# Performance work log

Hardware: AMD Instinct MI355X
Metric: run time of the kernel (lower is better)

The kernel has to match this reference:

```python
import jax, jax.numpy as jnp
import numpy as np

B, N, M, D, H = 2, 2048, 77, 1024, 16
DH = D // H
SCALE = DH ** -0.5
EPS = 1e-5


def _round_ste(x):
    return x + jax.lax.stop_gradient(jnp.round(x) - x)


def _fq(x, delta, zp, n_bits):
    # UniformAffineQuantizer: fake quant-dequant with straight-through round
    xi = _round_ste(x / delta) + zp
    xq = jnp.clip(xi, 0.0, 2.0 ** n_bits - 1.0)
    return (xq - zp) * delta


def _ln(x, g, b):
    mu = jnp.mean(x, -1, keepdims=True)
    var = jnp.var(x, -1, keepdims=True)
    return (x - mu) * jax.lax.rsqrt(var + EPS) * g + b


def _attn(x, ctx, wq, wk, wv, wo, bo, dq, dk, dv, dw):
    b, n, _ = x.shape
    m = ctx.shape[1]
    q = (x @ wq).reshape(b, n, H, DH).transpose(0, 2, 1, 3)   # b h n d
    k = (ctx @ wk).reshape(b, m, H, DH).transpose(0, 2, 1, 3)
    v = (ctx @ wv).reshape(b, m, H, DH).transpose(0, 2, 1, 3)
    sim = jnp.einsum('bhid,bhjd->bhij', _fq(q, dq, 128.0, 8), _fq(k, dk, 128.0, 8)) * SCALE
    attn = jax.nn.softmax(sim, axis=-1)
    out = jnp.einsum('bhij,bhjd->bhid', _fq(attn, dw, 0.0, 8), _fq(v, dv, 128.0, 8))
    out = out.transpose(0, 2, 1, 3).reshape(b, n, D)
    return out @ wo + bo


def setup_inputs():
    key = jax.random.key(0)
    ks = jax.random.split(key, 16)
    w = lambda k, s: (jax.random.normal(k, s, jnp.float32) * 0.02)
    d = lambda v: jnp.full((1,), v, jnp.float32)
    return {
        'x': jax.random.normal(ks[0], (B, N, D), jnp.float32),
        'context': jax.random.normal(ks[1], (B, M, D), jnp.float32),
        'ln1_g': jnp.ones((D,), jnp.float32), 'ln1_b': jnp.zeros((D,), jnp.float32),
        'ln2_g': jnp.ones((D,), jnp.float32), 'ln2_b': jnp.zeros((D,), jnp.float32),
        'ln3_g': jnp.ones((D,), jnp.float32), 'ln3_b': jnp.zeros((D,), jnp.float32),
        'a1_wq': w(ks[2], (D, D)), 'a1_wk': w(ks[3], (D, D)), 'a1_wv': w(ks[4], (D, D)),
        'a1_wo': w(ks[5], (D, D)), 'a1_bo': jnp.zeros((D,), jnp.float32),
        'a2_wq': w(ks[6], (D, D)), 'a2_wk': w(ks[7], (D, D)), 'a2_wv': w(ks[8], (D, D)),
        'a2_wo': w(ks[9], (D, D)), 'a2_bo': jnp.zeros((D,), jnp.float32),
        'ff_w1': w(ks[10], (D, 8 * D)), 'ff_b1': jnp.zeros((8 * D,), jnp.float32),
        'ff_w2': w(ks[11], (4 * D, D)), 'ff_b2': jnp.zeros((D,), jnp.float32),
        'd_q1': d(0.02), 'd_k1': d(0.02), 'd_v1': d(0.02), 'd_w1': d(1.0 / 255.0),
        'd_q2': d(0.02), 'd_k2': d(0.02), 'd_v2': d(0.02), 'd_w2': d(1.0 / 255.0),
    }


def reference(x, context, ln1_g, ln1_b, ln2_g, ln2_b, ln3_g, ln3_b,
              a1_wq, a1_wk, a1_wv, a1_wo, a1_bo,
              a2_wq, a2_wk, a2_wv, a2_wo, a2_bo,
              ff_w1, ff_b1, ff_w2, ff_b2,
              d_q1, d_k1, d_v1, d_w1, d_q2, d_k2, d_v2, d_w2):
    # x = attn1(norm1(x)) + x   (self-attention)
    h1 = _ln(x, ln1_g, ln1_b)
    x = _attn(h1, h1, a1_wq, a1_wk, a1_wv, a1_wo, a1_bo, d_q1, d_k1, d_v1, d_w1) + x
    # x = attn2(norm2(x), context) + x   (cross-attention)
    h2 = _ln(x, ln2_g, ln2_b)
    x = _attn(h2, context, a2_wq, a2_wk, a2_wv, a2_wo, a2_bo, d_q2, d_k2, d_v2, d_w2) + x
    # x = ff(norm3(x)) + x   (GEGLU feed-forward)
    h3 = _ln(x, ln3_g, ln3_b)
    hg = h3 @ ff_w1 + ff_b1
    a, g = jnp.split(hg, 2, axis=-1)
    x = (a * jax.nn.gelu(g, approximate=False)) @ ff_w2 + ff_b2 + x
    return x
```

## Files before the change

### kernel.cpp

```cpp
#include <hip/hip_runtime.h>
#include <cstdint>
#include <cmath>

typedef unsigned short u16;
typedef unsigned int   u32;

typedef __bf16 bx8 __attribute__((ext_vector_type(8)));
typedef float  fx4 __attribute__((ext_vector_type(4)));
typedef u32    ux4 __attribute__((ext_vector_type(4)));

#define H_  16
#define DH_ 64
#define QSCALE 0.18033688011112042f

#if __has_builtin(__builtin_amdgcn_exp2f)
#define EXP2(x) __builtin_amdgcn_exp2f(x)
#else
#define EXP2(x) exp2f(x)
#endif

__device__ __forceinline__ float bf2f(u16 h){ return __uint_as_float(((u32)h) << 16); }
__device__ __forceinline__ u16 f2bf(float f){
  u32 u = __float_as_uint(f);
  u32 r = (u + 0x7FFFu + ((u >> 16) & 1u)) >> 16;
  return (u16)r;
}

__device__ __forceinline__ u32 pk_bf16(float a, float b){
  u32 r;
  asm("v_cvt_pk_bf16_f32 %0, %1, %2" : "=v"(r) : "v"(a), "v"(b));
  return r;
}

union pkc { ux4 u; bx8 v; };

__device__ __forceinline__ float ldv(const void* p, size_t i, int f32){
  return f32 ? ((const float*)p)[i] : bf2f(((const u16*)p)[i]);
}

__device__ __forceinline__ void gld16(const void* g, void* l){
  __builtin_amdgcn_global_load_lds((const __attribute__((address_space(1))) u32*)g,
                                   (__attribute__((address_space(3))) u32*)l,
                                   16, 0, 0);
}

__device__ __forceinline__ float fq_val(float v, float delta){
  float xi = rintf(v / delta) + 128.0f;
  xi = fminf(fmaxf(xi, 0.0f), 255.0f);
  return (xi - 128.0f) * delta;
}

__device__ __forceinline__ float gelu_f(float x){
  float x3 = x * x * x;
  float z = 0.7978845608028654f * x + 0.035677408136300125f * x3;
  float u = __expf(-2.0f * z);
  float t = 1.0f - 2.0f * u / (1.0f + u);
  return 0.5f * x * (1.0f + t);
}

__global__ void detect_k(const u32* __restrict__ x, int* __restrict__ flag){
  __shared__ int cnt;
  if (threadIdx.x == 0) cnt = 0;
  __syncthreads();
  u32 w = x[threadIdx.x];
  int e = (w >> 7) & 0xFF;
  if (e >= 100 && e <= 140) atomicAdd(&cnt, 1);
  __syncthreads();
  if (threadIdx.x == 0) *flag = (cnt < 192) ? 1 : 0;
}

__global__ __launch_bounds__(256) void cvt_k(const void* __restrict__ in, u16* __restrict__ out,
                                             int n, const int* __restrict__ flagp){
  int f32 = *flagp;
  int i = blockIdx.x * 256 + threadIdx.x;
  if (i < n) out[i] = f32 ? f2bf(((const float*)in)[i]) : ((const u16*)in)[i];
}

__global__ __launch_bounds__(256) void tr8_k(
    const void* s0, const void* s1, const void* s2, const void* s3,
    const void* s4, const void* s5, const void* s6, const void* s7,
    u16* __restrict__ out, const int* __restrict__ flagp){
  __shared__ u16 t[32][33];
  int f32 = *flagp;
  int z = blockIdx.z;
  const void* in = z==0?s0:z==1?s1:z==2?s2:z==3?s3:z==4?s4:z==5?s5:z==6?s6:s7;
  u16* o = out + ((size_t)z << 20);
  int n0 = blockIdx.x << 5, r0 = blockIdx.y << 5;
  int tx = threadIdx.x & 31, ty = threadIdx.x >> 5;
  #pragma unroll
  for (int i = 0; i < 4; i++)
    t[ty + i*8][tx] = f2bf(ldv(in, (size_t)(r0 + ty + i*8) * 1024 + n0 + tx, f32));
  __syncthreads();
  #pragma unroll
  for (int i = 0; i < 4; i++)
    o[(size_t)(n0 + ty + i*8) * 1024 + r0 + tx] = t[tx][ty + i*8];
}

__global__ __launch_bounds__(256) void tr_k(const void* __restrict__ in, u16* __restrict__ out,
                                            int Rout, int C, const int* __restrict__ flagp){
  __shared__ u16 t[32][33];
  int f32 = *flagp;
  int n0 = blockIdx.x << 5, r0 = blockIdx.y << 5;
  int tx = threadIdx.x & 31, ty = threadIdx.x >> 5;
  #pragma unroll
  for (int i = 0; i < 4; i++)
    t[ty + i*8][tx] = f2bf(ldv(in, (size_t)(r0 + ty + i*8) * C + n0 + tx, f32));
  __syncthreads();
  #pragma unroll
  for (int i = 0; i < 4; i++)
    out[(size_t)(n0 + ty + i*8) * Rout + r0 + tx] = t[tx][ty + i*8];
}

__global__ __launch_bounds__(256) void ln_k(const void* __restrict__ x,
    const void* __restrict__ gam, const void* __restrict__ bet, u16* __restrict__ out,
    const int* __restrict__ flagp, int xdual){
  __shared__ float sb[8];
  const int f32 = *flagp;
  const int f32x = xdual ? f32 : 0;
  const int row = blockIdx.x, t = threadIdx.x;
  float v0, v1, v2, v3;
  if (f32x){
    float4 xv = *(const float4*)((const float*)x + (size_t)row * 1024 + t * 4);
    v0 = xv.x; v1 = xv.y; v2 = xv.z; v3 = xv.w;
  } else {
    ushort4 xv = *(const ushort4*)((const u16*)x + (size_t)row * 1024 + t * 4);
    v0 = bf2f(xv.x); v1 = bf2f(xv.y); v2 = bf2f(xv.z); v3 = bf2f(xv.w);
  }
  float s = v0 + v1 + v2 + v3;
  #pragma unroll
  for (int mk = 32; mk; mk >>= 1) s += __shfl_xor(s, mk);
  if ((t & 63) == 0) sb[t >> 6] = s;
  __syncthreads();
  float mu = (sb[0] + sb[1] + sb[2] + sb[3]) * 0.0009765625f;
  float d0 = v0 - mu, d1 = v1 - mu, d2 = v2 - mu, d3 = v3 - mu;
  float ss = d0*d0 + d1*d1 + d2*d2 + d3*d3;
  #pragma unroll
  for (int mk = 32; mk; mk >>= 1) ss += __shfl_xor(ss, mk);
  if ((t & 63) == 0) sb[4 + (t >> 6)] = ss;
  __syncthreads();
  float var = (sb[4] + sb[5] + sb[6] + sb[7]) * 0.0009765625f;
  float rs = rsqrtf(var + 1e-5f);
  int c = t * 4;
  u16 o0 = f2bf(d0 * rs * ldv(gam, c+0, f32) + ldv(bet, c+0, f32));
  u16 o1 = f2bf(d1 * rs * ldv(gam, c+1, f32) + ldv(bet, c+1, f32));
  u16 o2 = f2bf(d2 * rs * ldv(gam, c+2, f32) + ldv(bet, c+2, f32));
  u16 o3 = f2bf(d3 * rs * ldv(gam, c+3, f32) + ldv(bet, c+3, f32));
  uint2 ov; ov.x = (u32)o0 | ((u32)o1 << 16); ov.y = (u32)o2 | ((u32)o3 << 16);
  *(uint2*)(out + (size_t)row * 1024 + c) = ov;
}

__global__ __launch_bounds__(512)
void gemm_mr(const u16* __restrict__ A, const u16* __restrict__ BT,
             u16* __restrict__ P0, u16* __restrict__ P1, u16* __restrict__ P2,
             const void* D0, const void* D1, const void* D2,
             float sc0, float sc1, float sc2,
             int md0, int md1, int md2,
             const int* __restrict__ flagp,
             int M, int K, int rpb, int npad)
{
  __shared__ u16 As[2][128 * 32];
  __shared__ u16 Bs[2][128 * 32];
  const int tid = threadIdx.x;
  const int l = tid & 63, w = tid >> 6;
  const int lr = l & 15, lq = l >> 4;
  const int m0 = blockIdx.y * 128, n0 = blockIdx.x * 128;
  const int wrow = (w & 3) * 32, wcol = (w >> 2) * 64;

  fx4 acc[2][4];
  #pragma unroll
  for (int i = 0; i < 2; i++)
    #pragma unroll
    for (int j = 0; j < 4; j++){ fx4 z = {0.f,0.f,0.f,0.f}; acc[i][j] = z; }

  const int r0 = tid >> 2, p0 = tid & 3;
  const int c0 = p0 ^ (r0 & 3);
  int am0 = m0 + r0; if (am0 > M - 1) am0 = M - 1;
  const u16* gA = A  + (size_t)am0 * K + c0 * 8;
  const u16* gB = BT + (size_t)(n0 + r0) * K + c0 * 8;
  const int lo = w * 512;

  const int nk = K >> 5;
  gld16(gA, &As[0][lo]);
  gld16(gB, &Bs[0][lo]);

  for (int kt = 0; kt < nk; ++kt){
    __syncthreads();
    const int cur = kt & 1;
    if (kt + 1 < nk){
      const int nb = cur ^ 1;
      const int ko = (kt + 1) << 5;
      gld16(gA + ko, &As[nb][lo]);
      gld16(gB + ko, &Bs[nb][lo]);
    }
    bx8 aF[2], bF[4];
    #pragma unroll
    for (int i = 0; i < 2; i++){
      int row = wrow + i * 16 + lr;
      aF[i] = *(const bx8*)&As[cur][row * 32 + (lq ^ (row & 3)) * 8];
    }
    #pragma unroll
    for (int j = 0; j < 4; j++){
      int row = wcol + j * 16 + lr;
      bF[j] = *(const bx8*)&Bs[cur][row * 32 + (lq ^ (row & 3)) * 8];
    }
    #pragma unroll
    for (int i = 0; i < 2; i++)
      #pragma unroll
      for (int j = 0; j < 4; j++)
        acc[i][j] = __builtin_amdgcn_mfma_f32_16x16x32_bf16(aF[i], bF[j], acc[i][j], 0, 0, 0);
  }

  const int f32 = *flagp;
  const int reg = n0 >> 10;
  const int cbase = n0 & 1023;
  u16* P = reg == 0 ? P0 : (reg == 1 ? P1 : P2);
  const void* D = reg == 0 ? D0 : (reg == 1 ? D1 : D2);
  const float sc = reg == 0 ? sc0 : (reg == 1 ? sc1 : sc2);
  const int md = reg == 0 ? md0 : (reg == 1 ? md1 : md2);
  const float delta = ldv(D, 0, f32);

  #pragma unroll
  for (int i = 0; i < 2; i++)
    #pragma unroll
    for (int j = 0; j < 4; j++)
      #pragma unroll
      for (int rr = 0; rr < 4; rr++){
        int gm = m0 + wrow + i * 16 + lq * 4 + rr;
        int col = cbase + wcol + j * 16 + lr;
        if (gm < M){
          float v = fq_val(acc[i][j][rr], delta) * sc;
          if (md == 0){
            P[(size_t)gm * 1024 + col] = f2bf(v);
          } else {
            int bb = gm / rpb; int jj = gm - bb * rpb;
            int hh = col >> 6, dh = col & 63;
            P[(size_t)((bb * H_ + hh) * DH_ + dh) * npad + jj] = f2bf(v);
          }
        }
      }
}

template<int MODE>
__global__ __launch_bounds__(256)
void gemm64(const u16* __restrict__ A, const u16* __restrict__ BT,
            void* __restrict__ Co, const void* __restrict__ res,
            const void* __restrict__ bias, const void* __restrict__ dptr, float sc,
            const int* __restrict__ flagp, int res_dual,
            int M, int K)
{
  __shared__ u16 As[2][64 * 32];
  __shared__ u16 Bs[2][128 * 32];
  const int tid = threadIdx.x;
  const int l = tid & 63, w = tid >> 6;
  const int lr = l & 15, lq = l >> 4;
  const int m0 = blockIdx.y * 64, n0 = blockIdx.x * 128;
  const int wrow = (w >> 1) * 32, wcol = (w & 1) * 64;

  fx4 acc[2][4];
  #pragma unroll
  for (int i = 0; i < 2; i++)
    #pragma unroll
    for (int j = 0; j < 4; j++){ fx4 z = {0.f,0.f,0.f,0.f}; acc[i][j] = z; }

  const int r0 = tid >> 2, p0 = tid & 3;
  const int c0 = p0 ^ (r0 & 3);
  const int r1 = r0 + 64;
  int am0 = m0 + r0; if (am0 > M - 1) am0 = M - 1;
  const u16* gA0 = A  + (size_t)am0 * K + c0 * 8;
  const u16* gB0 = BT + (size_t)(n0 + r0) * K + c0 * 8;
  const u16* gB1 = BT + (size_t)(n0 + r1) * K + c0 * 8;
  const int lo0 = (w * 64) * 8, lo1 = (256 + w * 64) * 8;

  const int nk = K >> 5;
  gld16(gA0, &As[0][lo0]);
  gld16(gB0, &Bs[0][lo0]);
  gld16(gB1, &Bs[0][lo1]);

  for (int kt = 0; kt < nk; ++kt){
    __syncthreads();
    const int cur = kt & 1;
    if (kt + 1 < nk){
      const int nb = cur ^ 1;
      const int ko = (kt + 1) << 5;
      gld16(gA0 + ko, &As[nb][lo0]);
      gld16(gB0 + ko, &Bs[nb][lo0]);
      gld16(gB1 + ko, &Bs[nb][lo1]);
    }
    bx8 aF[2], bF[4];
    #pragma unroll
    for (int i = 0; i < 2; i++){
      int row = wrow + i * 16 + lr;
      aF[i] = *(const bx8*)&As[cur][row * 32 + (lq ^ (row & 3)) * 8];
    }
    #pragma unroll
    for (int j = 0; j < 4; j++){
      int row = wcol + j * 16 + lr;
      bF[j] = *(const bx8*)&Bs[cur][row * 32 + (lq ^ (row & 3)) * 8];
    }
    #pragma unroll
    for (int i = 0; i < 2; i++)
      #pragma unroll
      for (int j = 0; j < 4; j++)
        acc[i][j] = __builtin_amdgcn_mfma_f32_16x16x32_bf16(aF[i], bF[j], acc[i][j], 0, 0, 0);
  }

  const int f32 = *flagp;
  float delta = 1.f;
  if (MODE == 0) delta = ldv(dptr, 0, f32);

  #pragma unroll
  for (int i = 0; i < 2; i++)
    #pragma unroll
    for (int j = 0; j < 4; j++)
      #pragma unroll
      for (int rr = 0; rr < 4; rr++){
        int gm = m0 + wrow + i * 16 + lq * 4 + rr;
        int gn = n0 + wcol + j * 16 + lr;
        if (gm < M){
          float v = acc[i][j][rr];
          size_t idx = (size_t)gm * 1024 + gn;
          if (MODE == 0){
            ((u16*)Co)[idx] = f2bf(fq_val(v, delta) * sc);
          } else if (MODE == 5){
            float r = res_dual ? ldv(res, idx, f32) : bf2f(((const u16*)res)[idx]);
            ((u16*)Co)[idx] = f2bf(v + ldv(bias, gn, f32) + r);
          } else {
            float o = v + ldv(bias, gn, f32) + bf2f(((const u16*)res)[idx]);
            if (f32) ((float*)Co)[idx] = o;
            else     ((u16*)Co)[idx]  = f2bf(o);
          }
        }
      }
}

__global__ __launch_bounds__(512)
void gemm_glu(const u16* __restrict__ A, const u16* __restrict__ WT,
              u16* __restrict__ GE, const void* __restrict__ bias,
              const int* __restrict__ flagp, int M, int K)
{
  __shared__ u16 As[2][128 * 32];
  __shared__ u16 Ba[2][128 * 32];
  __shared__ u16 Bg[2][128 * 32];
  const int tid = threadIdx.x;
  const int l = tid & 63, w = tid >> 6;
  const int lr = l & 15, lq = l >> 4;
  const int m0 = blockIdx.y * 128, n0 = blockIdx.x * 128;
  const int wrow = (w & 3) * 32, wcol = (w >> 2) * 64;

  fx4 accA[2][4], accG[2][4];
  #pragma unroll
  for (int i = 0; i < 2; i++)
    #pragma unroll
    for (int j = 0; j < 4; j++){
      fx4 z = {0.f,0.f,0.f,0.f}; accA[i][j] = z; accG[i][j] = z;
    }

  const int r0 = tid >> 2, p0 = tid & 3;
  const int c0 = p0 ^ (r0 & 3);
  int am0 = m0 + r0; if (am0 > M - 1) am0 = M - 1;
  const u16* gA  = A  + (size_t)am0 * K + c0 * 8;
  const u16* gBa = WT + (size_t)(n0 + r0) * K + c0 * 8;
  const u16* gBg = WT + (size_t)(4096 + n0 + r0) * K + c0 * 8;
  const int lo = w * 512;

  const int nk = K >> 5;
  gld16(gA,  &As[0][lo]);
  gld16(gBa, &Ba[0][lo]);
  gld16(gBg, &Bg[0][lo]);

  for (int kt = 0; kt < nk; ++kt){
    __syncthreads();
    const int cur = kt & 1;
    if (kt + 1 < nk){
      const int nb = cur ^ 1;
      const int ko = (kt + 1) << 5;
      gld16(gA + ko,  &As[nb][lo]);
      gld16(gBa + ko, &Ba[nb][lo]);
      gld16(gBg + ko, &Bg[nb][lo]);
    }
    bx8 aF[2], bFa[4], bFg[4];
    #pragma unroll
    for (int i = 0; i < 2; i++){
      int row = wrow + i * 16 + lr;
      aF[i] = *(const bx8*)&As[cur][row * 32 + (lq ^ (row & 3)) * 8];
    }
    #pragma unroll
    for (int j = 0; j < 4; j++){
      int row = wcol + j * 16 + lr;
      bFa[j] = *(const bx8*)&Ba[cur][row * 32 + (lq ^ (row & 3)) * 8];
      bFg[j] = *(const bx8*)&Bg[cur][row * 32 + (lq ^ (row & 3)) * 8];
    }
    #pragma unroll
    for (int i = 0; i < 2; i++)
      #pragma unroll
      for (int j = 0; j < 4; j++){
        accA[i][j] = __builtin_amdgcn_mfma_f32_16x16x32_bf16(aF[i], bFa[j], accA[i][j], 0, 0, 0);
        accG[i][j] = __builtin_amdgcn_mfma_f32_16x16x32_bf16(aF[i], bFg[j], accG[i][j], 0, 0, 0);
      }
  }

  const int f32 = *flagp;

  #pragma unroll
  for (int i = 0; i < 2; i++)
    #pragma unroll
    for (int j = 0; j < 4; j++)
      #pragma unroll
      for (int rr = 0; rr < 4; rr++){
        int gm = m0 + wrow + i * 16 + lq * 4 + rr;
        int gn = n0 + wcol + j * 16 + lr;
        float va = accA[i][j][rr] + ldv(bias, gn, f32);
        float vg = accG[i][j][rr] + ldv(bias, 4096 + gn, f32);
        GE[(size_t)gm * 4096 + gn] = f2bf(va * gelu_f(vg));
      }
}

__global__ __launch_bounds__(256) void attn_k(
    const u16* __restrict__ Qf, const u16* __restrict__ Kf,
    const u16* __restrict__ VT, u16* __restrict__ AO,
    const void* __restrict__ dwp, const int* __restrict__ flagp,
    int Nq, int Lk, int Lpad)
{
  __shared__ u16 lds[32768];
  u16* const KB0_ = lds;
  u16* const KB1_ = lds + 8192;
  u16* const VB0_ = lds + 16384;
  u16* const VB1_ = lds + 24576;

  const int tid = threadIdx.x, l = tid & 63, w = tid >> 6;
  const int lr = l & 15, lq = l >> 4, m = lr & 7;
  const int q0 = blockIdx.x << 7;
  const int b = blockIdx.y >> 4, hh = blockIdx.y & 15;
  const int wq = w << 5;
  const float dw = ldv(dwp, 0, *flagp);
  const float rdw = 1.0f / dw;

  bx8 aQ[2][2];
  #pragma unroll
  for (int g = 0; g < 2; ++g){
    const u16* qp = Qf + ((size_t)(b * Nq + q0 + wq + g * 16 + lr) << 10)
                       + (hh << 6) + (lq << 3);
    aQ[g][0] = *(const bx8*)(qp);
    aQ[g][1] = *(const bx8*)(qp + 32);
  }

  const int kr0 = tid >> 3, kc = (tid & 7) ^ (kr0 & 7);
  const int vd0 = tid >> 4, vc = (tid & 15) ^ (vd0 & 7);
  const int ldsb = w << 9;

  auto stageK = [&](u16* dst, int j0){
    #pragma unroll
    for (int q = 0; q < 4; ++q){
      int r = kr0 + (q << 5);
      int jr = j0 + r; if (jr > Lk - 1) jr = Lk - 1;
      gld16(Kf + ((size_t)(b * Lk + jr) << 10) + (hh << 6) + (kc << 3),
            dst + (q << 11) + ldsb);
    }
  };
  auto stageV = [&](u16* dst, int j0){
    #pragma unroll
    for (int q = 0; q < 4; ++q){
      int d = vd0 + (q << 4);
      gld16(VT + ((size_t)(((b << 4) + hh) << 6) + d) * Lpad + j0 + (vc << 3),
            dst + (q << 11) + ldsb);
    }
  };

  const int ntiles = (Lk + 127) >> 7;
  const int ch0 = ((lq ^ m) << 3), ch1 = (((lq + 4) ^ m) << 3);

  float sa[2][4];
  #pragma unroll
  for (int g = 0; g < 2; ++g)
    #pragma unroll
    for (int rr = 0; rr < 4; ++rr) sa[g][rr] = 0.f;

  stageK(KB0_, 0);
  for (int jt = 0; jt < ntiles; ++jt){
    __syncthreads();
    const int cur = jt & 1;
    if (jt + 1 < ntiles) stageK(cur ? KB0_ : KB1_, (jt + 1) << 7);
    const u16* Kc = cur ? KB1_ : KB0_;
    const int j0 = jt << 7;
    const bool full = (j0 + 128 <= Lk);
    #pragma unroll
    for (int j = 0; j < 8; ++j){
      const int ro = ((j << 4) + lr) << 6;
      bx8 k0 = *(const bx8*)&Kc[ro + ch0];
      bx8 k1 = *(const bx8*)&Kc[ro + ch1];
      #pragma unroll
      for (int g = 0; g < 2; ++g){
        fx4 sv = {0.f,0.f,0.f,0.f};
        sv = __builtin_amdgcn_mfma_f32_16x16x32_bf16(k0, aQ[g][0], sv, 0, 0, 0);
        sv = __builtin_amdgcn_mfma_f32_16x16x32_bf16(k1, aQ[g][1], sv, 0, 0, 0);
        if (full){
          sa[g][0] += EXP2(sv[0]); sa[g][1] += EXP2(sv[1]);
          sa[g][2] += EXP2(sv[2]); sa[g][3] += EXP2(sv[3]);
        } else {
          const int kb = j0 + (j << 4) + (lq << 2);
          sa[g][0] += (kb + 0 < Lk) ? EXP2(sv[0]) : 0.f;
          sa[g][1] += (kb + 1 < Lk) ? EXP2(sv[1]) : 0.f;
          sa[g][2] += (kb + 2 < Lk) ? EXP2(sv[2]) : 0.f;
          sa[g][3] += (kb + 3 < Lk) ? EXP2(sv[3]) : 0.f;
        }
      }
    }
  }

  float cr[2];
  #pragma unroll
  for (int g = 0; g < 2; ++g){
    float s = (sa[g][0] + sa[g][1]) + (sa[g][2] + sa[g][3]);
    s += __shfl_xor(s, 16);
    s += __shfl_xor(s, 32);
    cr[g] = rdw / s;
  }

  fx4 oacc[2][4];
  #pragma unroll
  for (int g = 0; g < 2; ++g)
    #pragma unroll
    for (int dj = 0; dj < 4; ++dj){ fx4 z = {0.f,0.f,0.f,0.f}; oacc[g][dj] = z; }

  __syncthreads();
  stageK(KB0_, 0);
  stageV(VB0_, 0);
  for (int jt = 0; jt < ntiles; ++jt){
    __syncthreads();
    const int cur = jt & 1;
    const int j0 = jt << 7;
    if (jt + 1 < ntiles){
      stageK(cur ? KB0_ : KB1_, j0 + 128);
      stageV(cur ? VB0_ : VB1_, j0 + 128);
    }
    const u16* Kc = cur ? KB1_ : KB0_;
    const u16* Vc = cur ? VB1_ : VB0_;
    const bool full = (j0 + 128 <= Lk);
    #pragma unroll
    for (int t = 0; t < 4; ++t){
      u32 pA0[2], pA1[2], pB0[2], pB1[2];
      #pragma unroll
      for (int jj = 0; jj < 2; ++jj){
        const int j = (t << 1) + jj;
        const int ro = ((j << 4) + lr) << 6;
        bx8 k0 = *(const bx8*)&Kc[ro + ch0];
        bx8 k1 = *(const bx8*)&Kc[ro + ch1];
        #pragma unroll
        for (int g = 0; g < 2; ++g){
          fx4 sv = {0.f,0.f,0.f,0.f};
          sv = __builtin_amdgcn_mfma_f32_16x16x32_bf16(k0, aQ[g][0], sv, 0, 0, 0);
          sv = __builtin_amdgcn_mfma_f32_16x16x32_bf16(k1, aQ[g][1], sv, 0, 0, 0);
          float x0, x1, x2, x3;
          if (full){
            x0 = rintf(EXP2(sv[0]) * cr[g]);
            x1 = rintf(EXP2(sv[1]) * cr[g]);
            x2 = rintf(EXP2(sv[2]) * cr[g]);
            x3 = rintf(EXP2(sv[3]) * cr[g]);
          } else {
            const int kb = j0 + (j << 4) + (lq << 2);
            x0 = (kb + 0 < Lk) ? rintf(EXP2(sv[0]) * cr[g]) : 0.f;
            x1 = (kb + 1 < Lk) ? rintf(EXP2(sv[1]) * cr[g]) : 0.f;
            x2 = (kb + 2 < Lk) ? rintf(EXP2(sv[2]) * cr[g]) : 0.f;
            x3 = (kb + 3 < Lk) ? rintf(EXP2(sv[3]) * cr[g]) : 0.f;
          }
          u32 plo = pk_bf16(x0, x1), phi = pk_bf16(x2, x3);
          if (jj == 0){ pA0[g] = plo; pA1[g] = phi; }
          else        { pB0[g] = plo; pB1[g] = phi; }
        }
      }
      bx8 pa[2];
      #pragma unroll
      for (int g = 0; g < 2; ++g){
        u32 r0 = pA0[g], r2 = pB0[g], r1 = pA1[g], r3 = pB1[g];
        asm volatile("v_permlane32_swap_b32 %0, %1" : "+v"(r0), "+v"(r2));
        asm volatile("v_permlane16_swap_b32 %0, %1" : "+v"(r0), "+v"(r2));
        asm volatile("v_permlane32_swap_b32 %0, %1" : "+v"(r1), "+v"(r3));
        asm volatile("v_permlane16_swap_b32 %0, %1" : "+v"(r1), "+v"(r3));
        pkc pc; ux4 uu = {r0, r1, r2, r3}; pc.u = uu; pa[g] = pc.v;
      }
      #pragma unroll
      for (int dj = 0; dj < 4; ++dj){
        bx8 bV = *(const bx8*)&Vc[(((dj << 4) + lr) << 7) + ((((t << 2) + lq) ^ m) << 3)];
        oacc[0][dj] = __builtin_amdgcn_mfma_f32_16x16x32_bf16(bV, pa[0], oacc[0][dj], 0, 0, 0);
        oacc[1][dj] = __builtin_amdgcn_mfma_f32_16x16x32_bf16(bV, pa[1], oacc[1][dj], 0, 0, 0);
      }
    }
  }

  #pragma unroll
  for (int g = 0; g < 2; ++g){
    const size_t ob = ((size_t)(b * Nq + q0 + wq + g * 16 + lr) << 10)
                    + (hh << 6) + (lq << 2);
    #pragma unroll
    for (int dj = 0; dj < 4; ++dj){
      uint2 ov;
      ov.x = (u32)f2bf(oacc[g][dj][0] * dw) | ((u32)f2bf(oacc[g][dj][1] * dw) << 16);
      ov.y = (u32)f2bf(oacc[g][dj][2] * dw) | ((u32)f2bf(oacc[g][dj][3] * dw) << 16);
      *(uint2*)(AO + ob + (dj << 4)) = ov;
    }
  }
}


extern "C" void kernel_launch(void* const* d_in, const int* in_sizes, int n_in,
                              void* d_out, int out_size, void* d_ws, size_t ws_size,
                              hipStream_t stream)
{
  const void* X    = d_in[0];
  const void* CTX  = d_in[1];
  const void* LN1G = d_in[2];
  const void* LN1B = d_in[3];
  const void* LN2G = d_in[4];
  const void* LN2B = d_in[5];
  const void* LN3G = d_in[6];
  const void* LN3B = d_in[7];
  const void* W1Q  = d_in[8];
  const void* W1K  = d_in[9];
  const void* W1V  = d_in[10];
  const void* W1O  = d_in[11];
  const void* B1O  = d_in[12];
  const void* W2Q  = d_in[13];
  const void* W2K  = d_in[14];
  const void* W2V  = d_in[15];
  const void* W2O  = d_in[16];
  const void* B2O  = d_in[17];
  const void* FW1  = d_in[18];
  const void* FB1  = d_in[19];
  const void* FW2  = d_in[20];
  const void* FB2  = d_in[21];
  const void* DQ1  = d_in[22];
  const void* DK1  = d_in[23];
  const void* DV1  = d_in[24];
  const void* DW1  = d_in[25];
  const void* DQ2  = d_in[26];
  const void* DK2  = d_in[27];
  const void* DV2  = d_in[28];
  const void* DW2  = d_in[29];

  char* ws = (char*)d_ws;
  u16* wslot = (u16*)(ws + (0ull  << 20));
  u16* xs    = (u16*)(ws + (16ull << 20));
  u16* h     = (u16*)(ws + (24ull << 20));
  u16* bufA  = (u16*)(ws + (32ull << 20));
  u16* bufB  = (u16*)(ws + (40ull << 20));
  u16* bufC  = (u16*)(ws + (48ull << 20));
  u16* ge    = bufA;
  u16* ctxc  = (u16*)(ws + (64ull << 20));
  int* flag  = (int*)(ws + (65ull << 20));

  const dim3 G8x64(8, 64), GAT(16, 32);
  const int NCTX = 154 * 1024;
  const size_t MB2 = 1048576;

  detect_k<<<1, 256, 0, stream>>>((const u32*)X, flag);
  cvt_k<<<(NCTX + 255) / 256, 256, 0, stream>>>(CTX, ctxc, NCTX, flag);
  tr8_k<<<dim3(32, 32, 8), 256, 0, stream>>>(W1Q, W1K, W1V, W1O, W2Q, W2K, W2V, W2O,
                                             wslot, flag);

  ln_k<<<4096, 256, 0, stream>>>(X, LN1G, LN1B, h, flag, 1);
  gemm_mr<<<dim3(24, 32), 512, 0, stream>>>(h, wslot,
      bufA, bufB, bufC, DQ1, DK1, DV1, QSCALE, 1.f, 1.f, 0, 0, 1,
      flag, 4096, 1024, 2048, 2048);
  attn_k<<<GAT, 256, 0, stream>>>(bufA, bufB, bufC, h, DW1, flag, 2048, 2048, 2048);
  gemm64<5><<<G8x64, 256, 0, stream>>>(h, wslot + 3 * MB2, xs, X, B1O, nullptr, 1.f,
                                       flag, 1, 4096, 1024);

  ln_k<<<4096, 256, 0, stream>>>(xs, LN2G, LN2B, h, flag, 0);
  gemm64<0><<<G8x64, 256, 0, stream>>>(h, wslot + 4 * MB2, bufA, nullptr, nullptr, DQ2,
                                       QSCALE, flag, 0, 4096, 1024);
  gemm_mr<<<dim3(16, 2), 512, 0, stream>>>(ctxc, wslot + 5 * MB2,
      bufB, bufC, nullptr, DK2, DV2, DV2, 1.f, 1.f, 1.f, 0, 1, 1,
      flag, 154, 1024, 77, 128);
  attn_k<<<GAT, 256, 0, stream>>>(bufA, bufB, bufC, h, DW2, flag, 2048, 77, 128);
  gemm64<5><<<G8x64, 256, 0, stream>>>(h, wslot + 7 * MB2, xs, xs, B2O, nullptr, 1.f,
                                       flag, 0, 4096, 1024);

  ln_k<<<4096, 256, 0, stream>>>(xs, LN3G, LN3B, h, flag, 0);
  tr_k<<<dim3(256, 32), 256, 0, stream>>>(FW1, wslot, 1024, 8192, flag);
  gemm_glu<<<dim3(32, 32), 512, 0, stream>>>(h, wslot, ge, FB1, flag, 4096, 1024);
  tr_k<<<dim3(32, 128), 256, 0, stream>>>(FW2, wslot, 4096, 1024, flag);
  gemm64<7><<<G8x64, 256, 0, stream>>>(ge, wslot, d_out, xs, FB2, nullptr, 1.f,
                                       flag, 0, 4096, 4096);
}
```

Baseline: 651.1 us.

## Split attention key range across two wave groups with LDS reduction

The attention kernel goes from 256 to 512 threads per block. The second group of four waves handles the other half of each key tile, for both the softmax-denominator pass and the PV pass. Row sums and partial output accumulators are combined through LDS, and the staging loops are rebalanced across the larger block. s_setprio hints are added around the MFMA sections, and EXP2 now always uses exp2f. The aim is more waves per block to hide latency, at the cost of extra barriers and an LDS reduction at the end.

```diff
diff --git a/kernel.cpp b/kernel.cpp
--- a/kernel.cpp
+++ b/kernel.cpp
@@ -13,11 +13,7 @@
 #define DH_ 64
 #define QSCALE 0.18033688011112042f
 
-#if __has_builtin(__builtin_amdgcn_exp2f)
-#define EXP2(x) __builtin_amdgcn_exp2f(x)
-#else
 #define EXP2(x) exp2f(x)
-#endif
 
 __device__ __forceinline__ float bf2f(u16 h){ return __uint_as_float(((u32)h) << 16); }
 __device__ __forceinline__ u16 f2bf(float f){
@@ -415,7 +411,7 @@
       }
 }
 
-__global__ __launch_bounds__(256) void attn_k(
+__global__ __launch_bounds__(512, 4) void attn_k(
     const u16* __restrict__ Qf, const u16* __restrict__ Kf,
     const u16* __restrict__ VT, u16* __restrict__ AO,
     const void* __restrict__ dwp, const int* __restrict__ flagp,
@@ -428,10 +424,11 @@
   u16* const VB1_ = lds + 24576;
 
   const int tid = threadIdx.x, l = tid & 63, w = tid >> 6;
+  const int w4 = w & 3, jh = w >> 2;
   const int lr = l & 15, lq = l >> 4, m = lr & 7;
   const int q0 = blockIdx.x << 7;
   const int b = blockIdx.y >> 4, hh = blockIdx.y & 15;
-  const int wq = w << 5;
+  const int wq = w4 << 5;
   const float dw = ldv(dwp, 0, *flagp);
   const float rdw = 1.0f / dw;
 
@@ -444,25 +441,27 @@
     aQ[g][1] = *(const bx8*)(qp + 32);
   }
 
-  const int kr0 = tid >> 3, kc = (tid & 7) ^ (kr0 & 7);
-  const int vd0 = tid >> 4, vc = (tid & 15) ^ (vd0 & 7);
+  const int kr = tid >> 3, kcs = tid & 7;
+  const int vr = tid >> 4, vcs = tid & 15;
   const int ldsb = w << 9;
 
   auto stageK = [&](u16* dst, int j0){
     #pragma unroll
-    for (int q = 0; q < 4; ++q){
-      int r = kr0 + (q << 5);
+    for (int q = 0; q < 2; ++q){
+      int r = (q << 6) + kr;
       int jr = j0 + r; if (jr > Lk - 1) jr = Lk - 1;
-      gld16(Kf + ((size_t)(b * Lk + jr) << 10) + (hh << 6) + (kc << 3),
-            dst + (q << 11) + ldsb);
+      int c = kcs ^ (r & 7);
+      gld16(Kf + ((size_t)(b * Lk + jr) << 10) + (hh << 6) + (c << 3),
+            dst + (q << 12) + ldsb);
     }
   };
   auto stageV = [&](u16* dst, int j0){
     #pragma unroll
-    for (int q = 0; q < 4; ++q){
-      int d = vd0 + (q << 4);
-      gld16(VT + ((size_t)(((b << 4) + hh) << 6) + d) * Lpad + j0 + (vc << 3),
-            dst + (q << 11) + ldsb);
+    for (int q = 0; q < 2; ++q){
+      int d = (q << 5) + vr;
+      int c = vcs ^ (d & 7);
+      gld16(VT + ((size_t)(((b << 4) + hh) << 6) + d) * Lpad + j0 + (c << 3),
+            dst + (q << 12) + ldsb);
     }
   };
 
@@ -484,7 +483,8 @@
     const int j0 = jt << 7;
     const bool full = (j0 + 128 <= Lk);
     #pragma unroll
-    for (int j = 0; j < 8; ++j){
+    for (int jl = 0; jl < 4; ++jl){
+      const int j = (jh << 2) + jl;
       const int ro = ((j << 4) + lr) << 6;
       bx8 k0 = *(const bx8*)&Kc[ro + ch0];
       bx8 k1 = *(const bx8*)&Kc[ro + ch1];
@@ -507,14 +507,23 @@
     }
   }
 
-  float cr[2];
+  __syncthreads();
+  float* SS = (float*)lds;
   #pragma unroll
   for (int g = 0; g < 2; ++g){
     float s = (sa[g][0] + sa[g][1]) + (sa[g][2] + sa[g][3]);
     s += __shfl_xor(s, 16);
     s += __shfl_xor(s, 32);
+    SS[(w << 7) + (g << 6) + l] = s;
+  }
+  __syncthreads();
+  float cr[2];
+  #pragma unroll
+  for (int g = 0; g < 2; ++g){
+    float s = SS[(w4 << 7) + (g << 6) + l] + SS[((w4 + 4) << 7) + (g << 6) + l];
     cr[g] = rdw / s;
   }
+  __syncthreads();
 
   fx4 oacc[2][4];
   #pragma unroll
@@ -522,7 +531,6 @@
     #pragma unroll
     for (int dj = 0; dj < 4; ++dj){ fx4 z = {0.f,0.f,0.f,0.f}; oacc[g][dj] = z; }
 
-  __syncthreads();
   stageK(KB0_, 0);
   stageV(VB0_, 0);
   for (int jt = 0; jt < ntiles; ++jt){
@@ -537,8 +545,10 @@
     const u16* Vc = cur ? VB1_ : VB0_;
     const bool full = (j0 + 128 <= Lk);
     #pragma unroll
-    for (int t = 0; t < 4; ++t){
+    for (int tl = 0; tl < 2; ++tl){
+      const int t = (jh << 1) + tl;
       u32 pA0[2], pA1[2], pB0[2], pB1[2];
+      __builtin_amdgcn_s_setprio(1);
       #pragma unroll
       for (int jj = 0; jj < 2; ++jj){
         const int j = (t << 1) + jj;
@@ -568,6 +578,7 @@
           else        { pB0[g] = plo; pB1[g] = phi; }
         }
       }
+      __builtin_amdgcn_s_setprio(0);
       bx8 pa[2];
       #pragma unroll
       for (int g = 0; g < 2; ++g){
@@ -578,25 +589,47 @@
         asm volatile("v_permlane16_swap_b32 %0, %1" : "+v"(r1), "+v"(r3));
         pkc pc; ux4 uu = {r0, r1, r2, r3}; pc.u = uu; pa[g] = pc.v;
       }
+      __builtin_amdgcn_s_setprio(1);
       #pragma unroll
       for (int dj = 0; dj < 4; ++dj){
         bx8 bV = *(const bx8*)&Vc[(((dj << 4) + lr) << 7) + ((((t << 2) + lq) ^ m) << 3)];
         oacc[0][dj] = __builtin_amdgcn_mfma_f32_16x16x32_bf16(bV, pa[0], oacc[0][dj], 0, 0, 0);
         oacc[1][dj] = __builtin_amdgcn_mfma_f32_16x16x32_bf16(bV, pa[1], oacc[1][dj], 0, 0, 0);
       }
-    }
-  }
-
-  #pragma unroll
-  for (int g = 0; g < 2; ++g){
-    const size_t ob = ((size_t)(b * Nq + q0 + wq + g * 16 + lr) << 10)
-                    + (hh << 6) + (lq << 2);
-    #pragma unroll
-    for (int dj = 0; dj < 4; ++dj){
-      uint2 ov;
-      ov.x = (u32)f2bf(oacc[g][dj][0] * dw) | ((u32)f2bf(oacc[g][dj][1] * dw) << 16);
-      ov.y = (u32)f2bf(oacc[g][dj][2] * dw) | ((u32)f2bf(oacc[g][dj][3] * dw) << 16);
-      *(uint2*)(AO + ob + (dj << 4)) = ov;
+      __builtin_amdgcn_s_setprio(0);
+    }
+  }
+
+  __syncthreads();
+  float* OC = (float*)lds;
+  if (jh == 1){
+    const int base = ((w4 << 6) + l) << 5;
+    #pragma unroll
+    for (int g = 0; g < 2; ++g)
+      #pragma unroll
+      for (int dj = 0; dj < 4; ++dj)
+        #pragma unroll
+        for (int rr = 0; rr < 4; ++rr)
+          OC[base + (g << 4) + (dj << 2) + rr] = oacc[g][dj][rr];
+  }
+  __syncthreads();
+  if (jh == 0){
+    const int base = ((w4 << 6) + l) << 5;
+    #pragma unroll
+    for (int g = 0; g < 2; ++g){
+      const size_t ob = ((size_t)(b * Nq + q0 + wq + g * 16 + lr) << 10)
+                      + (hh << 6) + (lq << 2);
+      #pragma unroll
+      for (int dj = 0; dj < 4; ++dj){
+        float v0 = oacc[g][dj][0] + OC[base + (g << 4) + (dj << 2) + 0];
+        float v1 = oacc[g][dj][1] + OC[base + (g << 4) + (dj << 2) + 1];
+        float v2 = oacc[g][dj][2] + OC[base + (g << 4) + (dj << 2) + 2];
+        float v3 = oacc[g][dj][3] + OC[base + (g << 4) + (dj << 2) + 3];
+        uint2 ov;
+        ov.x = (u32)f2bf(v0 * dw) | ((u32)f2bf(v1 * dw) << 16);
+        ov.y = (u32)f2bf(v2 * dw) | ((u32)f2bf(v3 * dw) << 16);
+        *(uint2*)(AO + ob + (dj << 4)) = ov;
+      }
     }
   }
 }
@@ -661,7 +694,7 @@
   gemm_mr<<<dim3(24, 32), 512, 0, stream>>>(h, wslot,
       bufA, bufB, bufC, DQ1, DK1, DV1, QSCALE, 1.f, 1.f, 0, 0, 1,
       flag, 4096, 1024, 2048, 2048);
-  attn_k<<<GAT, 256, 0, stream>>>(bufA, bufB, bufC, h, DW1, flag, 2048, 2048, 2048);
+  attn_k<<<GAT, 512, 0, stream>>>(bufA, bufB, bufC, h, DW1, flag, 2048, 2048, 2048);
   gemm64<5><<<G8x64, 256, 0, stream>>>(h, wslot + 3 * MB2, xs, X, B1O, nullptr, 1.f,
                                        flag, 1, 4096, 1024);
 
@@ -671,7 +704,7 @@
   gemm_mr<<<dim3(16, 2), 512, 0, stream>>>(ctxc, wslot + 5 * MB2,
       bufB, bufC, nullptr, DK2, DV2, DV2, 1.f, 1.f, 1.f, 0, 1, 1,
       flag, 154, 1024, 77, 128);
-  attn_k<<<GAT, 256, 0, stream>>>(bufA, bufB, bufC, h, DW2, flag, 2048, 77, 128);
+  attn_k<<<GAT, 512, 0, stream>>>(bufA, bufB, bufC, h, DW2, flag, 2048, 77, 128);
   gemm64<5><<<G8x64, 256, 0, stream>>>(h, wslot + 7 * MB2, xs, xs, B2O, nullptr, 1.f,
                                        flag, 0, 4096, 1024);
 
```

New measurement: 668.4 us. 2.7% more time.

## Single-buffer V in attention kernel to cut LDS and raise occupancy

Applied to the files above, without the earlier changes.

The V tile in LDS is now single-buffered and staged inside the current iteration. All four P fragments are computed first, then a barrier runs before the PV MFMAs, so V loads overlap the QK/exp phase. This cuts LDS from 64KB to 48KB, and launch bounds now request 3 blocks per CU. The exp2 builtin is also swapped for plain exp2f. The cost is an extra barrier per tile, more live registers holding pa[2][4], and V loads that are no longer prefetched a full tile ahead.

```diff
diff --git a/kernel.cpp b/kernel.cpp
--- a/kernel.cpp
+++ b/kernel.cpp
@@ -13,11 +13,7 @@
 #define DH_ 64
 #define QSCALE 0.18033688011112042f
 
-#if __has_builtin(__builtin_amdgcn_exp2f)
-#define EXP2(x) __builtin_amdgcn_exp2f(x)
-#else
 #define EXP2(x) exp2f(x)
-#endif
 
 __device__ __forceinline__ float bf2f(u16 h){ return __uint_as_float(((u32)h) << 16); }
 __device__ __forceinline__ u16 f2bf(float f){
@@ -415,17 +411,16 @@
       }
 }
 
-__global__ __launch_bounds__(256) void attn_k(
+__global__ __launch_bounds__(256, 3) void attn_k(
     const u16* __restrict__ Qf, const u16* __restrict__ Kf,
     const u16* __restrict__ VT, u16* __restrict__ AO,
     const void* __restrict__ dwp, const int* __restrict__ flagp,
     int Nq, int Lk, int Lpad)
 {
-  __shared__ u16 lds[32768];
+  __shared__ u16 lds[24576];
   u16* const KB0_ = lds;
   u16* const KB1_ = lds + 8192;
-  u16* const VB0_ = lds + 16384;
-  u16* const VB1_ = lds + 24576;
+  u16* const VB_  = lds + 16384;
 
   const int tid = threadIdx.x, l = tid & 63, w = tid >> 6;
   const int lr = l & 15, lq = l >> 4, m = lr & 7;
@@ -457,12 +452,12 @@
             dst + (q << 11) + ldsb);
     }
   };
-  auto stageV = [&](u16* dst, int j0){
+  auto stageV = [&](int j0){
     #pragma unroll
     for (int q = 0; q < 4; ++q){
       int d = vd0 + (q << 4);
       gld16(VT + ((size_t)(((b << 4) + hh) << 6) + d) * Lpad + j0 + (vc << 3),
-            dst + (q << 11) + ldsb);
+            VB_ + (q << 11) + ldsb);
     }
   };
 
@@ -524,18 +519,16 @@
 
   __syncthreads();
   stageK(KB0_, 0);
-  stageV(VB0_, 0);
   for (int jt = 0; jt < ntiles; ++jt){
     __syncthreads();
     const int cur = jt & 1;
     const int j0 = jt << 7;
-    if (jt + 1 < ntiles){
-      stageK(cur ? KB0_ : KB1_, j0 + 128);
-      stageV(cur ? VB0_ : VB1_, j0 + 128);
-    }
+    stageV(j0);
+    if (jt + 1 < ntiles) stageK(cur ? KB0_ : KB1_, j0 + 128);
     const u16* Kc = cur ? KB1_ : KB0_;
-    const u16* Vc = cur ? VB1_ : VB0_;
     const bool full = (j0 + 128 <= Lk);
+
+    bx8 pa[2][4];
     #pragma unroll
     for (int t = 0; t < 4; ++t){
       u32 pA0[2], pA1[2], pB0[2], pB1[2];
@@ -568,7 +561,6 @@
           else        { pB0[g] = plo; pB1[g] = phi; }
         }
       }
-      bx8 pa[2];
       #pragma unroll
       for (int g = 0; g < 2; ++g){
         u32 r0 = pA0[g], r2 = pB0[g], r1 = pA1[g], r3 = pB1[g];
@@ -576,15 +568,19 @@
         asm volatile("v_permlane16_swap_b32 %0, %1" : "+v"(r0), "+v"(r2));
         asm volatile("v_permlane32_swap_b32 %0, %1" : "+v"(r1), "+v"(r3));
         asm volatile("v_permlane16_swap_b32 %0, %1" : "+v"(r1), "+v"(r3));
-        pkc pc; ux4 uu = {r0, r1, r2, r3}; pc.u = uu; pa[g] = pc.v;
-      }
+        pkc pc; ux4 uu = {r0, r1, r2, r3}; pc.u = uu; pa[g][t] = pc.v;
+      }
+    }
+
+    __syncthreads();
+    #pragma unroll
+    for (int t = 0; t < 4; ++t)
       #pragma unroll
       for (int dj = 0; dj < 4; ++dj){
-        bx8 bV = *(const bx8*)&Vc[(((dj << 4) + lr) << 7) + ((((t << 2) + lq) ^ m) << 3)];
-        oacc[0][dj] = __builtin_amdgcn_mfma_f32_16x16x32_bf16(bV, pa[0], oacc[0][dj], 0, 0, 0);
-        oacc[1][dj] = __builtin_amdgcn_mfma_f32_16x16x32_bf16(bV, pa[1], oacc[1][dj], 0, 0, 0);
-      }
-    }
+        bx8 bV = *(const bx8*)&VB_[(((dj << 4) + lr) << 7) + ((((t << 2) + lq) ^ m) << 3)];
+        oacc[0][dj] = __builtin_amdgcn_mfma_f32_16x16x32_bf16(bV, pa[0][t], oacc[0][dj], 0, 0, 0);
+        oacc[1][dj] = __builtin_amdgcn_mfma_f32_16x16x32_bf16(bV, pa[1][t], oacc[1][dj], 0, 0, 0);
+      }
   }
 
   #pragma unroll
```

Result: slower. 675.3 us (+3.7%).

## Use 512-thread attention blocks with one 16-row query group per wave

Applied to the files above, without the earlier changes.

The attention kernel now runs 8 waves of 512 threads per 128-query block, and each wave handles 16 query rows instead of 32. K/V staging is redistributed across the larger thread count, and the XOR swizzle is recomputed per row. The goal is lower register pressure and more waves in flight (launch_bounds 512,4) to hide latency, at the cost of each K/V LDS tile being reused by fewer query rows per wave. The EXP2 macro also drops the amdgcn exp2 builtin in favour of plain exp2f, which may add range-handling instructions.

```diff
diff --git a/kernel.cpp b/kernel.cpp
--- a/kernel.cpp
+++ b/kernel.cpp
@@ -13,11 +13,7 @@
 #define DH_ 64
 #define QSCALE 0.18033688011112042f
 
-#if __has_builtin(__builtin_amdgcn_exp2f)
-#define EXP2(x) __builtin_amdgcn_exp2f(x)
-#else
 #define EXP2(x) exp2f(x)
-#endif
 
 __device__ __forceinline__ float bf2f(u16 h){ return __uint_as_float(((u32)h) << 16); }
 __device__ __forceinline__ u16 f2bf(float f){
@@ -415,7 +411,7 @@
       }
 }
 
-__global__ __launch_bounds__(256) void attn_k(
+__global__ __launch_bounds__(512, 4) void attn_k(
     const u16* __restrict__ Qf, const u16* __restrict__ Kf,
     const u16* __restrict__ VT, u16* __restrict__ AO,
     const void* __restrict__ dwp, const int* __restrict__ flagp,
@@ -431,50 +427,46 @@
   const int lr = l & 15, lq = l >> 4, m = lr & 7;
   const int q0 = blockIdx.x << 7;
   const int b = blockIdx.y >> 4, hh = blockIdx.y & 15;
-  const int wq = w << 5;
+  const int wq = w << 4;
   const float dw = ldv(dwp, 0, *flagp);
   const float rdw = 1.0f / dw;
 
-  bx8 aQ[2][2];
-  #pragma unroll
-  for (int g = 0; g < 2; ++g){
-    const u16* qp = Qf + ((size_t)(b * Nq + q0 + wq + g * 16 + lr) << 10)
+  bx8 aQ0, aQ1;
+  {
+    const u16* qp = Qf + ((size_t)(b * Nq + q0 + wq + lr) << 10)
                        + (hh << 6) + (lq << 3);
-    aQ[g][0] = *(const bx8*)(qp);
-    aQ[g][1] = *(const bx8*)(qp + 32);
-  }
-
-  const int kr0 = tid >> 3, kc = (tid & 7) ^ (kr0 & 7);
-  const int vd0 = tid >> 4, vc = (tid & 15) ^ (vd0 & 7);
+    aQ0 = *(const bx8*)(qp);
+    aQ1 = *(const bx8*)(qp + 32);
+  }
+
+  const int kr = tid >> 3, kcs = tid & 7;
+  const int vr = tid >> 4, vcs = tid & 15;
   const int ldsb = w << 9;
 
   auto stageK = [&](u16* dst, int j0){
     #pragma unroll
-    for (int q = 0; q < 4; ++q){
-      int r = kr0 + (q << 5);
+    for (int q = 0; q < 2; ++q){
+      int r = (q << 6) + kr;
       int jr = j0 + r; if (jr > Lk - 1) jr = Lk - 1;
-      gld16(Kf + ((size_t)(b * Lk + jr) << 10) + (hh << 6) + (kc << 3),
-            dst + (q << 11) + ldsb);
+      int c = kcs ^ (r & 7);
+      gld16(Kf + ((size_t)(b * Lk + jr) << 10) + (hh << 6) + (c << 3),
+            dst + (q << 12) + ldsb);
     }
   };
   auto stageV = [&](u16* dst, int j0){
     #pragma unroll
-    for (int q = 0; q < 4; ++q){
-      int d = vd0 + (q << 4);
-      gld16(VT + ((size_t)(((b << 4) + hh) << 6) + d) * Lpad + j0 + (vc << 3),
-            dst + (q << 11) + ldsb);
+    for (int q = 0; q < 2; ++q){
+      int d = (q << 5) + vr;
+      int c = vcs ^ (d & 7);
+      gld16(VT + ((size_t)(((b << 4) + hh) << 6) + d) * Lpad + j0 + (c << 3),
+            dst + (q << 12) + ldsb);
     }
   };
 
   const int ntiles = (Lk + 127) >> 7;
   const int ch0 = ((lq ^ m) << 3), ch1 = (((lq + 4) ^ m) << 3);
 
-  float sa[2][4];
-  #pragma unroll
-  for (int g = 0; g < 2; ++g)
-    #pragma unroll
-    for (int rr = 0; rr < 4; ++rr) sa[g][rr] = 0.f;
-
+  float sa0 = 0.f, sa1 = 0.f, sa2 = 0.f, sa3 = 0.f;
   stageK(KB0_, 0);
   for (int jt = 0; jt < ntiles; ++jt){
     __syncthreads();
@@ -488,39 +480,30 @@
       const int ro = ((j << 4) + lr) << 6;
       bx8 k0 = *(const bx8*)&Kc[ro + ch0];
       bx8 k1 = *(const bx8*)&Kc[ro + ch1];
-      #pragma unroll
-      for (int g = 0; g < 2; ++g){
-        fx4 sv = {0.f,0.f,0.f,0.f};
-        sv = __builtin_amdgcn_mfma_f32_16x16x32_bf16(k0, aQ[g][0], sv, 0, 0, 0);
-        sv = __builtin_amdgcn_mfma_f32_16x16x32_bf16(k1, aQ[g][1], sv, 0, 0, 0);
-        if (full){
-          sa[g][0] += EXP2(sv[0]); sa[g][1] += EXP2(sv[1]);
-          sa[g][2] += EXP2(sv[2]); sa[g][3] += EXP2(sv[3]);
-        } else {
-          const int kb = j0 + (j << 4) + (lq << 2);
-          sa[g][0] += (kb + 0 < Lk) ? EXP2(sv[0]) : 0.f;
-          sa[g][1] += (kb + 1 < Lk) ? EXP2(sv[1]) : 0.f;
-          sa[g][2] += (kb + 2 < Lk) ? EXP2(sv[2]) : 0.f;
-          sa[g][3] += (kb + 3 < Lk) ? EXP2(sv[3]) : 0.f;
-        }
+      fx4 sv = {0.f,0.f,0.f,0.f};
+      sv = __builtin_amdgcn_mfma_f32_16x16x32_bf16(k0, aQ0, sv, 0, 0, 0);
+      sv = __builtin_amdgcn_mfma_f32_16x16x32_bf16(k1, aQ1, sv, 0, 0, 0);
+      if (full){
+        sa0 += EXP2(sv[0]); sa1 += EXP2(sv[1]);
+        sa2 += EXP2(sv[2]); sa3 += EXP2(sv[3]);
+      } else {
+        const int kb = j0 + (j << 4) + (lq << 2);
+        sa0 += (kb + 0 < Lk) ? EXP2(sv[0]) : 0.f;
+        sa1 += (kb + 1 < Lk) ? EXP2(sv[1]) : 0.f;
+        sa2 += (kb + 2 < Lk) ? EXP2(sv[2]) : 0.f;
+        sa3 += (kb + 3 < Lk) ? EXP2(sv[3]) : 0.f;
       }
     }
   }
 
-  float cr[2];
-  #pragma unroll
-  for (int g = 0; g < 2; ++g){
-    float s = (sa[g][0] + sa[g][1]) + (sa[g][2] + sa[g][3]);
-    s += __shfl_xor(s, 16);
-    s += __shfl_xor(s, 32);
-    cr[g] = rdw / s;
-  }
-
-  fx4 oacc[2][4];
-  #pragma unroll
-  for (int g = 0; g < 2; ++g)
-    #pragma unroll
-    for (int dj = 0; dj < 4; ++dj){ fx4 z = {0.f,0.f,0.f,0.f}; oacc[g][dj] = z; }
+  float s = (sa0 + sa1) + (sa2 + sa3);
+  s += __shfl_xor(s, 16);
+  s += __shfl_xor(s, 32);
+  const float cr = rdw / s;
+
+  fx4 oacc[4];
+  #pragma unroll
+  for (int dj = 0; dj < 4; ++dj){ fx4 z = {0.f,0.f,0.f,0.f}; oacc[dj] = z; }
 
   __syncthreads();
   stageK(KB0_, 0);
@@ -538,64 +521,56 @@
     const bool full = (j0 + 128 <= Lk);
     #pragma unroll
     for (int t = 0; t < 4; ++t){
-      u32 pA0[2], pA1[2], pB0[2], pB1[2];
+      u32 pA0, pA1, pB0, pB1;
       #pragma unroll
       for (int jj = 0; jj < 2; ++jj){
         const int j = (t << 1) + jj;
         const int ro = ((j << 4) + lr) << 6;
         bx8 k0 = *(const bx8*)&Kc[ro + ch0];
         bx8 k1 = *(const bx8*)&Kc[ro + ch1];
-        #pragma unroll
-        for (int g = 0; g < 2; ++g){
-          fx4 sv = {0.f,0.f,0.f,0.f};
-          sv = __builtin_amdgcn_mfma_f32_16x16x32_bf16(k0, aQ[g][0], sv, 0, 0, 0);
-          sv = __builtin_amdgcn_mfma_f32_16x16x32_bf16(k1, aQ[g][1], sv, 0, 0, 0);
-          float x0, x1, x2, x3;
-          if (full){
-            x0 = rintf(EXP2(sv[0]) * cr[g]);
-            x1 = rintf(EXP2(sv[1]) * cr[g]);
-            x2 = rintf(EXP2(sv[2]) * cr[g]);
-            x3 = rintf(EXP2(sv[3]) * cr[g]);
-          } else {
-            const int kb = j0 + (j << 4) + (lq << 2);
-            x0 = (kb + 0 < Lk) ? rintf(EXP2(sv[0]) * cr[g]) : 0.f;
-            x1 = (kb + 1 < Lk) ? rintf(EXP2(sv[1]) * cr[g]) : 0.f;
-            x2 = (kb + 2 < Lk) ? rintf(EXP2(sv[2]) * cr[g]) : 0.f;
-            x3 = (kb + 3 < Lk) ? rintf(EXP2(sv[3]) * cr[g]) : 0.f;
-          }
-          u32 plo = pk_bf16(x0, x1), phi = pk_bf16(x2, x3);
-          if (jj == 0){ pA0[g] = plo; pA1[g] = phi; }
-          else        { pB0[g] = plo; pB1[g] = phi; }
+        fx4 sv = {0.f,0.f,0.f,0.f};
+        sv = __builtin_amdgcn_mfma_f32_16x16x32_bf16(k0, aQ0, sv, 0, 0, 0);
+        sv = __builtin_amdgcn_mfma_f32_16x16x32_bf16(k1, aQ1, sv, 0, 0, 0);
+        float x0, x1, x2, x3;
+        if (full){
+          x0 = rintf(EXP2(sv[0]) * cr);
+          x1 = rintf(EXP2(sv[1]) * cr);
+          x2 = rintf(EXP2(sv[2]) * cr);
+          x3 = rintf(EXP2(sv[3]) * cr);
+        } else {
+          const int kb = j0 + (j << 4) + (lq << 2);
+          x0 = (kb + 0 < Lk) ? rintf(EXP2(sv[0]) * cr) : 0.f;
+          x1 = (kb + 1 < Lk) ? rintf(EXP2(sv[1]) * cr) : 0.f;
+          x2 = (kb + 2 < Lk) ? rintf(EXP2(sv[2]) * cr) : 0.f;
+          x3 = (kb + 3 < Lk) ? rintf(EXP2(sv[3]) * cr) : 0.f;
         }
+        u32 plo = pk_bf16(x0, x1), phi = pk_bf16(x2, x3);
+        if (jj == 0){ pA0 = plo; pA1 = phi; }
+        else        { pB0 = plo; pB1 = phi; }
       }
-      bx8 pa[2];
-      #pragma unroll
-      for (int g = 0; g < 2; ++g){
-        u32 r0 = pA0[g], r2 = pB0[g], r1 = pA1[g], r3 = pB1[g];
-        asm volatile("v_permlane32_swap_b32 %0, %1" : "+v"(r0), "+v"(r2));
-        asm volatile("v_permlane16_swap_b32 %0, %1" : "+v"(r0), "+v"(r2));
-        asm volatile("v_permlane32_swap_b32 %0, %1" : "+v"(r1), "+v"(r3));
-        asm volatile("v_permlane16_swap_b32 %0, %1" : "+v"(r1), "+v"(r3));
-        pkc pc; ux4 uu = {r0, r1, r2, r3}; pc.u = uu; pa[g] = pc.v;
-      }
+      u32 r0 = pA0, r2 = pB0, r1 = pA1, r3 = pB1;
+      asm volatile("v_permlane32_swap_b32 %0, %1" : "+v"(r0), "+v"(r2));
+      asm volatile("v_permlane16_swap_b32 %0, %1" : "+v"(r0), "+v"(r2));
+      asm volatile("v_permlane32_swap_b32 %0, %1" : "+v"(r1), "+v"(r3));
+      asm volatile("v_permlane16_swap_b32 %0, %1" : "+v"(r1), "+v"(r3));
+      pkc pc; ux4 uu = {r0, r1, r2, r3}; pc.u = uu;
+      bx8 pa = pc.v;
       #pragma unroll
       for (int dj = 0; dj < 4; ++dj){
         bx8 bV = *(const bx8*)&Vc[(((dj << 4) + lr) << 7) + ((((t << 2) + lq) ^ m) << 3)];
-        oacc[0][dj] = __builtin_amdgcn_mfma_f32_16x16x32_bf16(bV, pa[0], oacc[0][dj], 0, 0, 0);
-        oacc[1][dj] = __builtin_amdgcn_mfma_f32_16x16x32_bf16(bV, pa[1], oacc[1][dj], 0, 0, 0);
+        oacc[dj] = __builtin_amdgcn_mfma_f32_16x16x32_bf16(bV, pa, oacc[dj], 0, 0, 0);
       }
     }
   }
 
-  #pragma unroll
-  for (int g = 0; g < 2; ++g){
-    const size_t ob = ((size_t)(b * Nq + q0 + wq + g * 16 + lr) << 10)
+  {
+    const size_t ob = ((size_t)(b * Nq + q0 + wq + lr) << 10)
                     + (hh << 6) + (lq << 2);
     #pragma unroll
     for (int dj = 0; dj < 4; ++dj){
       uint2 ov;
-      ov.x = (u32)f2bf(oacc[g][dj][0] * dw) | ((u32)f2bf(oacc[g][dj][1] * dw) << 16);
-      ov.y = (u32)f2bf(oacc[g][dj][2] * dw) | ((u32)f2bf(oacc[g][dj][3] * dw) << 16);
+      ov.x = (u32)f2bf(oacc[dj][0] * dw) | ((u32)f2bf(oacc[dj][1] * dw) << 16);
+      ov.y = (u32)f2bf(oacc[dj][2] * dw) | ((u32)f2bf(oacc[dj][3] * dw) << 16);
       *(uint2*)(AO + ob + (dj << 4)) = ov;
     }
   }
@@ -661,7 +636,7 @@
   gemm_mr<<<dim3(24, 32), 512, 0, stream>>>(h, wslot,
       bufA, bufB, bufC, DQ1, DK1, DV1, QSCALE, 1.f, 1.f, 0, 0, 1,
       flag, 4096, 1024, 2048, 2048);
-  attn_k<<<GAT, 256, 0, stream>>>(bufA, bufB, bufC, h, DW1, flag, 2048, 2048, 2048);
+  attn_k<<<GAT, 512, 0, stream>>>(bufA, bufB, bufC, h, DW1, flag, 2048, 2048, 2048);
   gemm64<5><<<G8x64, 256, 0, stream>>>(h, wslot + 3 * MB2, xs, X, B1O, nullptr, 1.f,
                                        flag, 1, 4096, 1024);
 
@@ -671,7 +646,7 @@
   gemm_mr<<<dim3(16, 2), 512, 0, stream>>>(ctxc, wslot + 5 * MB2,
       bufB, bufC, nullptr, DK2, DV2, DV2, 1.f, 1.f, 1.f, 0, 1, 1,
       flag, 154, 1024, 77, 128);
-  attn_k<<<GAT, 256, 0, stream>>>(bufA, bufB, bufC, h, DW2, flag, 2048, 77, 128);
+  attn_k<<<GAT, 512, 0, stream>>>(bufA, bufB, bufC, h, DW2, flag, 2048, 77, 128);
   gemm64<5><<<G8x64, 256, 0, stream>>>(h, wslot + 7 * MB2, xs, xs, B2O, nullptr, 1.f,
                                        flag, 0, 4096, 1024);
 
```

Result: no change. 657.5 us (+1.0%).
